# Kernel optimization log

Hardware: AMD Instinct MI355X
Metric: run time of the kernel (lower is better)

The kernel has to match this reference:

```python
import jax, jax.numpy as jnp
import numpy as np

N = 24000; E = 384000; NT = 3; IN = 128; HID = 32; ED = 64; NE = 5; FFN = 64; C = 16
HEADS = (8, 8, 1); ALPHA = 0.05; DAL = 2


def _lrelu(x, s):
    return jnp.where(x >= 0, x, s * x)


def _elu(x):
    return jnp.where(x > 0, x, jnp.expm1(x))


def _ln(x, g, b, eps=1e-5):
    m = x.mean(-1, keepdims=True)
    v = ((x - m) ** 2).mean(-1, keepdims=True)
    return (x - m) / jnp.sqrt(v + eps) * g + b


def _l2n(x, eps=1e-12):
    return x / jnp.maximum(jnp.linalg.norm(x, axis=1, keepdims=True), eps)


def _ta(h, src, dst, e_feat, edge_emb, W, We, al, ar, ae, bias, res_W, res_attn, act):
    # SimpleHGN-style heterogeneous graph attention layer (TALayer)
    Hh = al.shape[0]
    feat = (h @ W).reshape(N, Hh, HID)                       # [N,H,D]
    ee = (edge_emb[e_feat] @ We).reshape(E, Hh, ED)          # [E,H,ED]
    el = (feat * al).sum(-1)                                 # [N,H]
    er = (feat * ar).sum(-1)                                 # [N,H]
    lg = _lrelu(el[src] + er[dst] + (ee * ae).sum(-1), 0.2)  # [E,H]
    m = jax.ops.segment_max(lg, dst, num_segments=N)         # edge softmax over dst
    a = jnp.exp(lg - m[dst])
    a = a / jax.ops.segment_sum(a, dst, num_segments=N)[dst]
    if res_attn is not None:
        a = a * (1.0 - ALPHA) + res_attn * ALPHA             # residual attention carry-over
    rst = jax.ops.segment_sum(a[:, :, None] * feat[src], dst, num_segments=N)
    if res_W is not None:
        rst = rst + (h @ res_W).reshape(N, Hh, HID)
    rst = rst + bias
    if act:
        rst = _elu(rst)
    return rst, jax.lax.stop_gradient(a)


def forward(feats, fc_W, fc_b, ntype_emb, W_ntype,
            ta0_edge_emb, ta0_W, ta0_We, ta0_al, ta0_ar, ta0_ae, ta0_bias,
            ta1_edge_emb, ta1_W, ta1_We, ta1_al, ta1_ar, ta1_ae, ta1_bias, ta1_res_W,
            ta2_edge_emb, ta2_W, ta2_We, ta2_al, ta2_ar, ta2_ae, ta2_bias, ta2_res_W,
            da_ln1_g, da_ln1_b, da_Wq, da_bq, da_Wk, da_bk, da_Wv, da_bv, da_Wo, da_bo,
            da_ln2_g, da_ln2_b, da_W1, da_b1, da_W2, da_b2, final_W, logits_W,
            e_feat, node_type, src, dst):
    # per-node-type input projection + leaky_relu(0.01), concat over types -> [N,HID]
    h = _lrelu(jnp.einsum('tni,tio->tno', feats, fc_W) + fc_b[:, None, :], 0.01).reshape(N, HID)
    ntype_feat = (ntype_emb @ W_ntype)[node_type]            # [N,HID]
    h = h * ntype_feat
    h0, a0 = _ta(h, src, dst, e_feat, ta0_edge_emb, ta0_W, ta0_We, ta0_al, ta0_ar, ta0_ae, ta0_bias, None, None, True)
    h = h0.reshape(N, -1)
    h1, _ = _ta(h, src, dst, e_feat, ta1_edge_emb, ta1_W, ta1_We, ta1_al, ta1_ar, ta1_ae, ta1_bias, ta1_res_W, a0, True)
    h = h1.reshape(N, -1)
    hf, _ = _ta(h, src, dst, e_feat, ta2_edge_emb, ta2_W, ta2_We, ta2_al, ta2_ar, ta2_ae, ta2_bias, ta2_res_W, None, False)
    h_feat = hf.reshape(N, HID)
    # dim-wise transformer (DALayer stack): tokens = HID dims, channel = 1
    x = (h_feat * ntype_feat)[:, :, None]                    # [N,HID,1]
    for l in range(DAL):
        y = _ln(x, da_ln1_g[l], da_ln1_b[l])
        q = y @ da_Wq[l] + da_bq[l]
        k = y @ da_Wk[l] + da_bk[l]
        v = y @ da_Wv[l] + da_bv[l]
        att = jax.nn.softmax(jnp.einsum('nqd,nkd->nqk', q, k), axis=-1)  # scale=att_size**-0.5=1
        x = x + (jnp.einsum('nqk,nkd->nqd', att, v) @ da_Wo[l] + da_bo[l])
        y = _ln(x, da_ln2_g[l], da_ln2_b[l])
        x = x + (jax.nn.gelu(y @ da_W1[l] + da_b1[l], approximate=False) @ da_W2[l] + da_b2[l])
    h_dim = _l2n(x[:, :, 0])
    h_final = jnp.concatenate([_l2n(h_feat), h_dim], axis=1) @ final_W
    logits = jax.nn.relu(h_final) @ logits_W
    return logits / jnp.maximum(jnp.linalg.norm(logits, axis=1, keepdims=True), 1e-12)


def setup_inputs():
    key = jax.random.key(0)
    ks = iter(jax.random.split(key, 96))
    def rn(shape, s=0.1):
        return jax.random.normal(next(ks), shape, jnp.float32) * s
    inp = {}
    inp["feats"] = jax.random.normal(next(ks), (NT, N // NT, IN), jnp.float32)
    inp["e_feat"] = jax.random.randint(next(ks), (E,), 0, NE)
    inp["node_type"] = jax.random.randint(next(ks), (N,), 0, NT)
    inp["src"] = jax.random.randint(next(ks), (E,), 0, N)
    inp["dst"] = jax.random.randint(next(ks), (E,), 0, N)
    inp["fc_W"] = rn((NT, IN, HID)); inp["fc_b"] = rn((NT, HID))
    inp["ntype_emb"] = rn((NT, HID)); inp["W_ntype"] = rn((HID, HID))
    ins = (HID, HID * HEADS[0], HID * HEADS[1])
    for l in range(3):
        Hh = HEADS[l]; di = ins[l]; p = "ta%d_" % l
        inp[p + "edge_emb"] = rn((NE, ED))
        inp[p + "W"] = rn((di, Hh * HID))
        inp[p + "We"] = rn((ED, Hh * ED))
        inp[p + "al"] = rn((Hh, HID)); inp[p + "ar"] = rn((Hh, HID)); inp[p + "ae"] = rn((Hh, ED))
        inp[p + "bias"] = jnp.zeros((Hh, HID), jnp.float32)
        if l > 0:
            inp[p + "res_W"] = rn((di, Hh * HID))
    inp["da_ln1_g"] = jnp.ones((DAL, 1), jnp.float32); inp["da_ln1_b"] = jnp.zeros((DAL, 1), jnp.float32)
    inp["da_Wq"] = rn((DAL, 1, 1)); inp["da_bq"] = jnp.zeros((DAL, 1), jnp.float32)
    inp["da_Wk"] = rn((DAL, 1, 1)); inp["da_bk"] = jnp.zeros((DAL, 1), jnp.float32)
    inp["da_Wv"] = rn((DAL, 1, 1)); inp["da_bv"] = jnp.zeros((DAL, 1), jnp.float32)
    inp["da_Wo"] = rn((DAL, 1, 1)); inp["da_bo"] = jnp.zeros((DAL, 1), jnp.float32)
    inp["da_ln2_g"] = jnp.ones((DAL, 1), jnp.float32); inp["da_ln2_b"] = jnp.zeros((DAL, 1), jnp.float32)
    inp["da_W1"] = rn((DAL, 1, FFN)); inp["da_b1"] = jnp.zeros((DAL, FFN), jnp.float32)
    inp["da_W2"] = rn((DAL, FFN, 1)); inp["da_b2"] = jnp.zeros((DAL, 1), jnp.float32)
    inp["final_W"] = rn((2 * HID, HID))
    inp["logits_W"] = rn((HID, C))
    return inp


def reference(feats, fc_W, fc_b, ntype_emb, W_ntype,
              ta0_edge_emb, ta0_W, ta0_We, ta0_al, ta0_ar, ta0_ae, ta0_bias,
              ta1_edge_emb, ta1_W, ta1_We, ta1_al, ta1_ar, ta1_ae, ta1_bias, ta1_res_W,
              ta2_edge_emb, ta2_W, ta2_We, ta2_al, ta2_ar, ta2_ae, ta2_bias, ta2_res_W,
              da_ln1_g, da_ln1_b, da_Wq, da_bq, da_Wk, da_bk, da_Wv, da_bv, da_Wo, da_bo,
              da_ln2_g, da_ln2_b, da_W1, da_b1, da_W2, da_b2, final_W, logits_W,
              e_feat, node_type, src, dst):
    return forward(feats, fc_W, fc_b, ntype_emb, W_ntype,
                   ta0_edge_emb, ta0_W, ta0_We, ta0_al, ta0_ar, ta0_ae, ta0_bias,
                   ta1_edge_emb, ta1_W, ta1_We, ta1_al, ta1_ar, ta1_ae, ta1_bias, ta1_res_W,
                   ta2_edge_emb, ta2_W, ta2_We, ta2_al, ta2_ar, ta2_ae, ta2_bias, ta2_res_W,
                   da_ln1_g, da_ln1_b, da_Wq, da_bq, da_Wk, da_bk, da_Wv, da_bv, da_Wo, da_bo,
                   da_ln2_g, da_ln2_b, da_W1, da_b1, da_W2, da_b2, final_W, logits_W,
                   e_feat, node_type, src, dst)
```

## Files before the change

### kernel.cpp

```cpp
#include <hip/hip_runtime.h>
#include <math.h>

constexpr int kN = 24000;
constexpr int kE = 384000;
constexpr float kAlpha = 0.05f;

typedef unsigned int   u32;
typedef unsigned short u16;
typedef __attribute__((ext_vector_type(8))) short short8;
typedef __attribute__((ext_vector_type(4))) float float4v;

__device__ __forceinline__ float bf2f(u16 x) { return __uint_as_float(((u32)x) << 16); }
__device__ __forceinline__ u16 f2bf(float f) {
  u32 u = __float_as_uint(f);
  return (u16)((u + 0x7fffu + ((u >> 16) & 1u)) >> 16);
}

__global__ void __launch_bounds__(256) zero_ints_kernel(int* __restrict__ p, int n) {
  int i = blockIdx.x * 256 + threadIdx.x;
  if (i < n) p[i] = 0;
}

__global__ void __launch_bounds__(256) count_kernel(const int* __restrict__ dst,
                                                    int* __restrict__ counts) {
  int e = blockIdx.x * 256 + threadIdx.x;
  if (e < kE) atomicAdd(&counts[dst[e]], 1);
}

__global__ void __launch_bounds__(1024) scan_kernel(const int* __restrict__ counts,
                                                    int* __restrict__ row_start) {
  __shared__ int wsum[16];
  __shared__ int carry_s;
  int tid = threadIdx.x, lane = tid & 63, wid = tid >> 6;
  if (tid == 0) { carry_s = 0; row_start[0] = 0; }
  __syncthreads();
  for (int base = 0; base < kN; base += 1024) {
    int x = (base + tid < kN) ? counts[base + tid] : 0;
    #pragma unroll
    for (int off = 1; off < 64; off <<= 1) {
      int y = __shfl_up(x, off);
      if (lane >= off) x += y;
    }
    if (lane == 63) wsum[wid] = x;
    __syncthreads();
    if (tid < 16) {
      int wv = wsum[tid];
      #pragma unroll
      for (int off = 1; off < 16; off <<= 1) {
        int y = __shfl_up(wv, off);
        if (tid >= off) wv += y;
      }
      wsum[tid] = wv;
    }
    __syncthreads();
    int incl = x + carry_s + (wid > 0 ? wsum[wid - 1] : 0);
    if (base + tid < kN) row_start[base + tid + 1] = incl;
    __syncthreads();
    if (tid == 1023) carry_s = incl;
    __syncthreads();
  }
}

__global__ void __launch_bounds__(256) scatter_kernel(const int* __restrict__ dst,
                                                      const int* __restrict__ row_start,
                                                      int* __restrict__ cursor,
                                                      int* __restrict__ edge_ids) {
  int e = blockIdx.x * 256 + threadIdx.x;
  if (e < kE) {
    int n = dst[e];
    int pos = row_start[n] + atomicAdd(&cursor[n], 1);
    edge_ids[pos] = e;
  }
}

__global__ void __launch_bounds__(256) prepack_kernel(
    const float* __restrict__ W0, const float* __restrict__ al0, const float* __restrict__ ar0,
    const float* __restrict__ W1, const float* __restrict__ al1, const float* __restrict__ ar1,
    const float* __restrict__ rW1,
    const float* __restrict__ W2, const float* __restrict__ al2, const float* __restrict__ ar2,
    const float* __restrict__ rW2,
    u16* __restrict__ WT0, u16* __restrict__ WT1, u16* __restrict__ WT2,
    const float* __restrict__ ntype_emb, const float* __restrict__ W_ntype,
    const float* __restrict__ emb0, const float* __restrict__ We0, const float* __restrict__ ae0,
    const float* __restrict__ emb1, const float* __restrict__ We1, const float* __restrict__ ae1,
    const float* __restrict__ emb2, const float* __restrict__ We2, const float* __restrict__ ae2,
    const float* __restrict__ ln1_b, const float* __restrict__ Wv, const float* __restrict__ bv,
    const float* __restrict__ Wo, const float* __restrict__ bo,
    const float* __restrict__ ln2_b, const float* __restrict__ DW1, const float* __restrict__ Db1,
    const float* __restrict__ DW2, const float* __restrict__ Db2,
    float* __restrict__ ntf, float* __restrict__ eterm, float* __restrict__ dadelta) {
  __shared__ float wae[17][64];
  __shared__ float red[128];
  int tid = threadIdx.x;
  if (blockIdx.x < 744) {
    const int SZ0 = 10240, SZ1 = 576 * 256;
    int gid = blockIdx.x * 256 + tid;
    float v = 0.f;
    if (gid < 2048) {
      int n = gid / 32, k = gid % 32;
      if (n < 8)       { for (int d = 0; d < 32; ++d) v += W0[k * 256 + n * 32 + d] * al0[n * 32 + d]; }
      else if (n < 16) { int h = n - 8; for (int d = 0; d < 32; ++d) v += W0[k * 256 + h * 32 + d] * ar0[h * 32 + d]; }
      WT0[n * 32 + k] = f2bf(v);
    } else if (gid < SZ0) {
      int i = gid - 2048;
      int h = i >> 10, rem = i & 1023, d = rem >> 5, k = rem & 31;
      WT0[2048 + i] = f2bf(W0[k * 256 + h * 32 + d]);
    } else if (gid < SZ0 + SZ1) {
      int i = gid - SZ0;
      int n = i / 256, k = i % 256;
      if (n < 256) v = W1[k * 256 + n];
      else if (n < 264) { int h = n - 256; for (int d = 0; d < 32; ++d) v += W1[k * 256 + h * 32 + d] * al1[h * 32 + d]; }
      else if (n < 272) { int h = n - 264; for (int d = 0; d < 32; ++d) v += W1[k * 256 + h * 32 + d] * ar1[h * 32 + d]; }
      else if (n < 528) v = rW1[k * 256 + (n - 272)];
      WT1[n * 256 + k] = f2bf(v);
    } else {
      int i = gid - SZ0 - SZ1;
      int n = i / 256, k = i % 256;
      if (n < 32) v = W2[k * 32 + n];
      else if (n == 32) { for (int d = 0; d < 32; ++d) v += W2[k * 32 + d] * al2[d]; }
      else if (n == 33) { for (int d = 0; d < 32; ++d) v += W2[k * 32 + d] * ar2[d]; }
      else if (n < 66) v = rW2[k * 32 + (n - 34)];
      WT2[n * 256 + k] = f2bf(v);
    }
  } else {
    for (int idx = tid; idx < 17 * 64; idx += 256) {
      int hg = idx >> 6, k = idx & 63;
      const float* We; const float* ae; int Hh, h;
      if (hg < 8)       { We = We0; ae = ae0; Hh = 8; h = hg; }
      else if (hg < 16) { We = We1; ae = ae1; Hh = 8; h = hg - 8; }
      else              { We = We2; ae = ae2; Hh = 1; h = 0; }
      float s = 0.f;
      for (int d = 0; d < 64; ++d) s += We[(size_t)k * Hh * 64 + h * 64 + d] * ae[h * 64 + d];
      wae[hg][k] = s;
    }
    __syncthreads();
    for (int id = tid; id < 85; id += 256) {
      const float* emb; int Hh, t, h, hg, base;
      if (id < 40)      { emb = emb0; Hh = 8; t = id / 8;  h = id % 8; hg = h;      base = 0;  }
      else if (id < 80) { int i = id - 40; emb = emb1; Hh = 8; t = i / 8; h = i % 8; hg = 8 + h; base = 40; }
      else              { int i = id - 80; emb = emb2; Hh = 1; t = i;    h = 0;     hg = 16;    base = 80; }
      float s = 0.f;
      for (int k = 0; k < 64; ++k) s += emb[t * 64 + k] * wae[hg][k];
      eterm[base + t * Hh + h] = s;
    }
    for (int idx = tid; idx < 96; idx += 256) {
      int t = idx / 32, o = idx % 32;
      float s = 0.f;
      for (int k = 0; k < 32; ++k) s += ntype_emb[t * 32 + k] * W_ntype[k * 32 + o];
      ntf[idx] = s;
    }
    for (int i2 = tid; i2 < 128; i2 += 256) {
      int l = i2 >> 6, j = i2 & 63;
      float u = ln2_b[l] * DW1[l * 64 + j] + Db1[l * 64 + j];
      float g = 0.5f * u * (1.0f + erff(u * 0.7071067811865476f));
      red[i2] = g * DW2[l * 64 + j];
    }
    __syncthreads();
    if (tid == 0) {
      float delta = 0.f;
      for (int l = 0; l < 2; ++l) {
        float vs = ln1_b[l] * Wv[l] + bv[l];
        delta += vs * Wo[l] + bo[l] + Db2[l];
      }
      for (int i = 0; i < 128; ++i) delta += red[i];
      *dadelta = delta;
    }
  }
}

__global__ void __launch_bounds__(256) inproj_kernel(
    const float* __restrict__ feats, const float* __restrict__ fc_W,
    const float* __restrict__ fc_b, const float* __restrict__ ntf,
    const int* __restrict__ node_type, u16* __restrict__ hb) {
  int t = blockIdx.x * 256 + threadIdx.x;
  if (t >= kN * 32) return;
  int n = t >> 5, o = t & 31;
  int ty = n / 8000;
  const float* fr = &feats[(size_t)n * 128];
  const float* w  = &fc_W[(size_t)ty * 4096 + o];
  float s = fc_b[ty * 32 + o];
  #pragma unroll
  for (int k = 0; k < 128; k += 4) {
    float4 f = *(const float4*)&fr[k];
    s += f.x * w[(k + 0) * 32] + f.y * w[(k + 1) * 32]
       + f.z * w[(k + 2) * 32] + f.w * w[(k + 3) * 32];
  }
  s = (s < 0.f) ? 0.01f * s : s;
  hb[t] = f2bf(s * ntf[node_type[n] * 32 + o]);
}

template <int K>
__global__ void __launch_bounds__(256) mfma_gemm_kernel(
    const u16* __restrict__ A, const u16* __restrict__ WT,
    const float* __restrict__ bias,
    u16* __restrict__ featb, float* __restrict__ el, float* __restrict__ er,
    u16* __restrict__ resb, float* __restrict__ resf,
    int NT, int N1, int HH, int N2) {
  constexpr int RB = K * 2;
  constexpr int CPR = K / 8;
  __shared__ __align__(16) u16 As[64 * K];
  __shared__ __align__(16) u16 Bs[64 * K];
  const int tid = threadIdx.x;
  const int l = tid & 63;
  const int w = tid >> 6;
  const int wm = w >> 1, wn = w & 1;
  const int m0 = blockIdx.x * 64;
  const int kslot = l >> 4;
  const int l15 = l & 15;

  #pragma unroll
  for (int c = tid; c < 64 * CPR; c += 256) {
    int row = c / CPR, ch = c - row * CPR;
    int off = (row * RB + ch * 16) ^ ((row & 7) << 4);
    *(uint4*)((char*)As + off) = *(const uint4*)(A + (size_t)(m0 + row) * K + ch * 8);
  }

  for (int ct = 0; ct < NT; ++ct) {
    __syncthreads();
    #pragma unroll
    for (int c = tid; c < 64 * CPR; c += 256) {
      int row = c / CPR, ch = c - row * CPR;
      int off = (row * RB + ch * 16) ^ ((row & 7) << 4);
      *(uint4*)((char*)Bs + off) = *(const uint4*)(WT + (size_t)(ct * 64 + row) * K + ch * 8);
    }
    __syncthreads();

    float4v acc[2][2];
    #pragma unroll
    for (int f = 0; f < 2; ++f)
      #pragma unroll
      for (int g = 0; g < 2; ++g) { acc[f][g][0]=0.f; acc[f][g][1]=0.f; acc[f][g][2]=0.f; acc[f][g][3]=0.f; }

    #pragma unroll
    for (int kc = 0; kc < K; kc += 32) {
      short8 af[2], bf[2];
      #pragma unroll
      for (int f = 0; f < 2; ++f) {
        int row = wm * 32 + f * 16 + l15;
        int off = (row * RB + kc * 2 + kslot * 16) ^ ((row & 7) << 4);
        af[f] = *(const short8*)((const char*)As + off);
      }
      #pragma unroll
      for (int g = 0; g < 2; ++g) {
        int n = wn * 32 + g * 16 + l15;
        int off = (n * RB + kc * 2 + kslot * 16) ^ ((n & 7) << 4);
        bf[g] = *(const short8*)((const char*)Bs + off);
      }
      #pragma unroll
      for (int f = 0; f < 2; ++f)
        #pragma unroll
        for (int g = 0; g < 2; ++g)
          acc[f][g] = __builtin_amdgcn_mfma_f32_16x16x32_bf16(af[f], bf[g], acc[f][g], 0, 0, 0);
    }

    const int rbase = kslot * 4;
    #pragma unroll
    for (int f = 0; f < 2; ++f) {
      #pragma unroll
      for (int g = 0; g < 2; ++g) {
        int gc = ct * 64 + wn * 32 + g * 16 + l15;
        #pragma unroll
        for (int reg = 0; reg < 4; ++reg) {
          int gr = m0 + wm * 32 + f * 16 + rbase + reg;
          float v = acc[f][g][reg];
          if (gc < N1) {
            featb[(size_t)gr * N1 + gc] = f2bf(v);
          } else if (gc < N1 + HH) {
            el[(size_t)gr * HH + (gc - N1)] = v;
          } else if (gc < N1 + 2 * HH) {
            er[(size_t)gr * HH + (gc - N1 - HH)] = v;
          } else if (gc < N1 + 2 * HH + N2) {
            int c2 = gc - N1 - 2 * HH;
            float vv = v + bias[c2];
            if (resb) resb[(size_t)gr * N2 + c2] = f2bf(vv);
            else      resf[(size_t)gr * N2 + c2] = vv;
          }
        }
      }
    }
  }
}

__global__ void __launch_bounds__(256) agg8h_kernel(
    const int* __restrict__ row_start, const int* __restrict__ edge_ids,
    const int* __restrict__ src, const int* __restrict__ ef,
    const float* __restrict__ el, const float* __restrict__ er,
    const float* __restrict__ eterm,
    const u16* __restrict__ Hb,
    _Float16* __restrict__ a0h,
    u16* __restrict__ Gb) {
  int n = (blockIdx.x * 256 + threadIdx.x) >> 6;
  if (n >= kN) return;
  int l = threadIdx.x & 63;
  int h = l >> 3, s = l & 7;
  int s0 = row_start[n], s1 = row_start[n + 1];
  float ern = er[n * 8 + h];
  float et0 = eterm[0 * 8 + h], et1 = eterm[1 * 8 + h], et2 = eterm[2 * 8 + h];
  float et3 = eterm[3 * 8 + h], et4 = eterm[4 * 8 + h];
  float m = -1e30f, ssum = 0.f;
  for (int i = s0 + s; i < s1; i += 8) {
    int e = edge_ids[i];
    int efc = ef[e];
    float etv = (efc == 0) ? et0 : (efc == 1) ? et1 : (efc == 2) ? et2 : (efc == 3) ? et3 : et4;
    float lg = el[src[e] * 8 + h] + ern + etv;
    lg = (lg < 0.f) ? 0.2f * lg : lg;
    if (lg > m) { ssum = ssum * expf(m - lg) + 1.f; m = lg; }
    else        { ssum += expf(lg - m); }
  }
  #pragma unroll
  for (int mk = 1; mk <= 4; mk <<= 1) {
    float om = __shfl_xor(m, mk);
    float os = __shfl_xor(ssum, mk);
    float nm = fmaxf(m, om);
    ssum = ssum * expf(m - nm) + os * expf(om - nm);
    m = nm;
  }
  float inv = 1.f / ssum;
  float4 acc = make_float4(0.f, 0.f, 0.f, 0.f);
  int i = s0;
  for (; i + 8 <= s1; i += 8) {
    int e = edge_ids[i + s];
    int sek = src[e];
    int efc = ef[e];
    float etv = (efc == 0) ? et0 : (efc == 1) ? et1 : (efc == 2) ? et2 : (efc == 3) ? et3 : et4;
    float lg = el[sek * 8 + h] + ern + etv;
    lg = (lg < 0.f) ? 0.2f * lg : lg;
    float am = expf(lg - m) * inv;
    a0h[(size_t)e * 8 + h] = (_Float16)am;
    #pragma unroll
    for (int j = 0; j < 8; ++j) {
      float aj = __shfl(am, (h << 3) + j);
      int sej = __shfl(sek, j);
      ushort4 fv = *(const ushort4*)(Hb + (size_t)sej * 32 + s * 4);
      acc.x = fmaf(aj, bf2f(fv.x), acc.x);
      acc.y = fmaf(aj, bf2f(fv.y), acc.y);
      acc.z = fmaf(aj, bf2f(fv.z), acc.z);
      acc.w = fmaf(aj, bf2f(fv.w), acc.w);
    }
  }
  if (i < s1) {
    int cnt = s1 - i;
    float am = 0.f; int sek = 0;
    if (s < cnt) {
      int e = edge_ids[i + s];
      sek = src[e];
      int efc = ef[e];
      float etv = (efc == 0) ? et0 : (efc == 1) ? et1 : (efc == 2) ? et2 : (efc == 3) ? et3 : et4;
      float lg = el[sek * 8 + h] + ern + etv;
      lg = (lg < 0.f) ? 0.2f * lg : lg;
      am = expf(lg - m) * inv;
      a0h[(size_t)e * 8 + h] = (_Float16)am;
    }
    for (int j = 0; j < cnt; ++j) {
      float aj = __shfl(am, (h << 3) + j);
      int sej = __shfl(sek, j);
      ushort4 fv = *(const ushort4*)(Hb + (size_t)sej * 32 + s * 4);
      acc.x = fmaf(aj, bf2f(fv.x), acc.x);
      acc.y = fmaf(aj, bf2f(fv.y), acc.y);
      acc.z = fmaf(aj, bf2f(fv.z), acc.z);
      acc.w = fmaf(aj, bf2f(fv.w), acc.w);
    }
  }
  ushort4 pw;
  pw.x = f2bf(acc.x); pw.y = f2bf(acc.y); pw.z = f2bf(acc.z); pw.w = f2bf(acc.w);
  *(ushort4*)(Gb + (size_t)n * 256 + h * 32 + s * 4) = pw;
}

__global__ void __launch_bounds__(256) bd_gemm_kernel(
    const u16* __restrict__ Gb,
    const u16* __restrict__ WbdT,
    const float* __restrict__ bias,
    u16* __restrict__ outb) {
  __shared__ __align__(16) u16 As[64 * 256];
  __shared__ __align__(16) u16 Bs[8 * 32 * 32];
  const int tid = threadIdx.x;
  const int l = tid & 63;
  const int w = tid >> 6;
  const int m0 = blockIdx.x * 64;
  const int kslot = l >> 4, l15 = l & 15;
  for (int c = tid; c < 64 * 32; c += 256) {
    int row = c >> 5, ch = c & 31;
    int off = (row * 512 + ch * 16) ^ ((row & 7) << 4);
    *(uint4*)((char*)As + off) = *(const uint4*)(Gb + (size_t)(m0 + row) * 256 + ch * 8);
  }
  for (int c = tid; c < 256 * 4; c += 256) {
    int r = c >> 2, ch = c & 3;
    int off = (r * 64 + ch * 16) ^ ((r & 7) << 4);
    *(uint4*)((char*)Bs + off) = *(const uint4*)(WbdT + (size_t)r * 32 + ch * 8);
  }
  __syncthreads();
  #pragma unroll
  for (int hh = 0; hh < 2; ++hh) {
    int h = w * 2 + hh;
    short8 af[4];
    #pragma unroll
    for (int f = 0; f < 4; ++f) {
      int row = f * 16 + l15;
      int off = (row * 512 + h * 64 + kslot * 16) ^ ((row & 7) << 4);
      af[f] = *(const short8*)((const char*)As + off);
    }
    short8 bf[2];
    #pragma unroll
    for (int g = 0; g < 2; ++g) {
      int r = h * 32 + g * 16 + l15;
      int off = (r * 64 + kslot * 16) ^ ((r & 7) << 4);
      bf[g] = *(const short8*)((const char*)Bs + off);
    }
    #pragma unroll
    for (int f = 0; f < 4; ++f) {
      #pragma unroll
      for (int g = 0; g < 2; ++g) {
        float4v acc = {0.f, 0.f, 0.f, 0.f};
        acc = __builtin_amdgcn_mfma_f32_16x16x32_bf16(af[f], bf[g], acc, 0, 0, 0);
        #pragma unroll
        for (int reg = 0; reg < 4; ++reg) {
          int gr = m0 + f * 16 + kslot * 4 + reg;
          int gc = h * 32 + g * 16 + l15;
          float v = acc[reg] + bias[gc];
          v = (v > 0.f) ? v : expm1f(v);
          outb[(size_t)gr * 256 + gc] = f2bf(v);
        }
      }
    }
  }
}

__global__ void __launch_bounds__(256) agg8w_kernel(
    const int* __restrict__ row_start, const int* __restrict__ edge_ids,
    const int* __restrict__ src, const int* __restrict__ ef,
    const float* __restrict__ el, const float* __restrict__ er,
    const float* __restrict__ eterm,
    const u16* __restrict__ featb,
    const _Float16* __restrict__ a0h,
    const u16* __restrict__ accb,
    u16* __restrict__ outb) {
  int n = (blockIdx.x * 256 + threadIdx.x) >> 6;
  if (n >= kN) return;
  int l = threadIdx.x & 63;
  int h = l >> 3, s = l & 7;
  int s0 = row_start[n], s1 = row_start[n + 1];
  float ern = er[n * 8 + h];
  float et0 = eterm[0 * 8 + h], et1 = eterm[1 * 8 + h], et2 = eterm[2 * 8 + h];
  float et3 = eterm[3 * 8 + h], et4 = eterm[4 * 8 + h];
  float m = -1e30f, ssum = 0.f;
  for (int i = s0 + s; i < s1; i += 8) {
    int e = edge_ids[i];
    int efc = ef[e];
    float etv = (efc == 0) ? et0 : (efc == 1) ? et1 : (efc == 2) ? et2 : (efc == 3) ? et3 : et4;
    float lg = el[src[e] * 8 + h] + ern + etv;
    lg = (lg < 0.f) ? 0.2f * lg : lg;
    if (lg > m) { ssum = ssum * expf(m - lg) + 1.f; m = lg; }
    else        { ssum += expf(lg - m); }
  }
  #pragma unroll
  for (int mk = 1; mk <= 4; mk <<= 1) {
    float om = __shfl_xor(m, mk);
    float os = __shfl_xor(ssum, mk);
    float nm = fmaxf(m, om);
    ssum = ssum * expf(m - nm) + os * expf(om - nm);
    m = nm;
  }
  float inv = 1.f / ssum;
  const size_t rowoff = (size_t)n * 256 + h * 32 + s * 4;
  ushort4 rv = *(const ushort4*)(accb + rowoff);
  float4 acc = make_float4(bf2f(rv.x), bf2f(rv.y), bf2f(rv.z), bf2f(rv.w));
  int i = s0;
  for (; i + 8 <= s1; i += 8) {
    int e = edge_ids[i + s];
    int sek = src[e];
    int efc = ef[e];
    float etv = (efc == 0) ? et0 : (efc == 1) ? et1 : (efc == 2) ? et2 : (efc == 3) ? et3 : et4;
    float lg = el[sek * 8 + h] + ern + etv;
    lg = (lg < 0.f) ? 0.2f * lg : lg;
    float am = expf(lg - m) * inv;
    am = am * (1.f - kAlpha) + (float)a0h[(size_t)e * 8 + h] * kAlpha;
    #pragma unroll
    for (int j = 0; j < 8; ++j) {
      float aj = __shfl(am, (h << 3) + j);
      int sej = __shfl(sek, j);
      ushort4 fv = *(const ushort4*)(featb + (size_t)sej * 256 + h * 32 + s * 4);
      acc.x = fmaf(aj, bf2f(fv.x), acc.x);
      acc.y = fmaf(aj, bf2f(fv.y), acc.y);
      acc.z = fmaf(aj, bf2f(fv.z), acc.z);
      acc.w = fmaf(aj, bf2f(fv.w), acc.w);
    }
  }
  if (i < s1) {
    int cnt = s1 - i;
    float am = 0.f; int sek = 0;
    if (s < cnt) {
      int e = edge_ids[i + s];
      sek = src[e];
      int efc = ef[e];
      float etv = (efc == 0) ? et0 : (efc == 1) ? et1 : (efc == 2) ? et2 : (efc == 3) ? et3 : et4;
      float lg = el[sek * 8 + h] + ern + etv;
      lg = (lg < 0.f) ? 0.2f * lg : lg;
      am = expf(lg - m) * inv;
      am = am * (1.f - kAlpha) + (float)a0h[(size_t)e * 8 + h] * kAlpha;
    }
    for (int j = 0; j < cnt; ++j) {
      float aj = __shfl(am, (h << 3) + j);
      int sej = __shfl(sek, j);
      ushort4 fv = *(const ushort4*)(featb + (size_t)sej * 256 + h * 32 + s * 4);
      acc.x = fmaf(aj, bf2f(fv.x), acc.x);
      acc.y = fmaf(aj, bf2f(fv.y), acc.y);
      acc.z = fmaf(aj, bf2f(fv.z), acc.z);
      acc.w = fmaf(aj, bf2f(fv.w), acc.w);
    }
  }
  acc.x = (acc.x > 0.f) ? acc.x : expm1f(acc.x);
  acc.y = (acc.y > 0.f) ? acc.y : expm1f(acc.y);
  acc.z = (acc.z > 0.f) ? acc.z : expm1f(acc.z);
  acc.w = (acc.w > 0.f) ? acc.w : expm1f(acc.w);
  ushort4 pw;
  pw.x = f2bf(acc.x); pw.y = f2bf(acc.y); pw.z = f2bf(acc.z); pw.w = f2bf(acc.w);
  *(ushort4*)(outb + rowoff) = pw;
}

__global__ void __launch_bounds__(256) aggw1_final_kernel(
    const int* __restrict__ row_start, const int* __restrict__ edge_ids,
    const int* __restrict__ src, const int* __restrict__ ef,
    const float* __restrict__ el, const float* __restrict__ er,
    const float* __restrict__ eterm,
    const u16* __restrict__ featb,
    const float* __restrict__ S2,
    const float* __restrict__ ntf, const int* __restrict__ node_type,
    const float* __restrict__ dadelta,
    const float* __restrict__ finalW, const float* __restrict__ logitsW,
    float* __restrict__ out) {
  __shared__ float fWs[2048];
  __shared__ float lWs[512];
  __shared__ float abuf[8][32];
  __shared__ float bbuf[8][32];
  __shared__ float sbuf[8][32];
  const int tid = threadIdx.x;
  for (int i = tid; i < 2048; i += 256) fWs[i] = finalW[i];
  for (int i = tid; i < 512; i += 256) lWs[i] = logitsW[i];
  const int slot = tid >> 5;
  const int g = tid & 31;
  const int gb = tid & 32;
  const int n = blockIdx.x * 8 + slot;
  const int s0 = row_start[n], s1 = row_start[n + 1];
  float ern = er[n];
  float et0 = eterm[0], et1 = eterm[1], et2 = eterm[2], et3 = eterm[3], et4 = eterm[4];
  float m = -1e30f, ssum = 0.f;
  for (int i = s0 + g; i < s1; i += 32) {
    int e = edge_ids[i];
    int efc = ef[e];
    float etv = (efc == 0) ? et0 : (efc == 1) ? et1 : (efc == 2) ? et2 : (efc == 3) ? et3 : et4;
    float lg = el[src[e]] + ern + etv;
    lg = (lg < 0.f) ? 0.2f * lg : lg;
    if (lg > m) { ssum = ssum * expf(m - lg) + 1.f; m = lg; }
    else        { ssum += expf(lg - m); }
  }
  #pragma unroll
  for (int mk = 1; mk <= 16; mk <<= 1) {
    float om = __shfl_xor(m, mk);
    float os = __shfl_xor(ssum, mk);
    float nm = fmaxf(m, om);
    ssum = ssum * expf(m - nm) + os * expf(om - nm);
    m = nm;
  }
  float inv = 1.f / ssum;
  float acc = S2[(size_t)n * 32 + g];
  int i = s0;
  for (; i + 32 <= s1; i += 32) {
    int e = edge_ids[i + g];
    int sek = src[e];
    int efc = ef[e];
    float etv = (efc == 0) ? et0 : (efc == 1) ? et1 : (efc == 2) ? et2 : (efc == 3) ? et3 : et4;
    float lg = el[sek] + ern + etv;
    lg = (lg < 0.f) ? 0.2f * lg : lg;
    float am = expf(lg - m) * inv;
    #pragma unroll
    for (int j = 0; j < 32; ++j) {
      float aj = __shfl(am, gb + j);
      int sej = __shfl(sek, gb + j);
      acc = fmaf(aj, bf2f(featb[(size_t)sej * 32 + g]), acc);
    }
  }
  if (i < s1) {
    int cnt = s1 - i;
    float am = 0.f; int sek = 0;
    if (g < cnt) {
      int e = edge_ids[i + g];
      sek = src[e];
      int efc = ef[e];
      float etv = (efc == 0) ? et0 : (efc == 1) ? et1 : (efc == 2) ? et2 : (efc == 3) ? et3 : et4;
      float lg = el[sek] + ern + etv;
      lg = (lg < 0.f) ? 0.2f * lg : lg;
      am = expf(lg - m) * inv;
    }
    for (int j = 0; j < cnt; ++j) {
      float aj = __shfl(am, gb + j);
      int sej = __shfl(sek, gb + j);
      acc = fmaf(aj, bf2f(featb[(size_t)sej * 32 + g]), acc);
    }
  }
  float delta = dadelta[0];
  float ntv = ntf[node_type[n] * 32 + g];
  float av = acc;
  float bv = acc * ntv + delta;
  float na = av * av, nb = bv * bv;
  #pragma unroll
  for (int mk = 1; mk <= 16; mk <<= 1) {
    na += __shfl_xor(na, mk);
    nb += __shfl_xor(nb, mk);
  }
  float inva = 1.f / fmaxf(sqrtf(na), 1e-12f);
  float invb = 1.f / fmaxf(sqrtf(nb), 1e-12f);
  __syncthreads();
  abuf[slot][g] = av * inva;
  bbuf[slot][g] = bv * invb;
  __syncthreads();
  float s = 0.f;
  #pragma unroll
  for (int d = 0; d < 32; ++d)
    s += abuf[slot][d] * fWs[d * 32 + g] + bbuf[slot][d] * fWs[(32 + d) * 32 + g];
  s = fmaxf(s, 0.f);
  sbuf[slot][g] = s;
  __syncthreads();
  if (g < 16) {
    float lg = 0.f;
    #pragma unroll
    for (int o = 0; o < 32; ++o) lg += sbuf[slot][o] * lWs[o * 16 + g];
    float nl = lg * lg;
    #pragma unroll
    for (int mk = 1; mk <= 8; mk <<= 1) nl += __shfl_xor(nl, mk);
    float invl = 1.f / fmaxf(sqrtf(nl), 1e-12f);
    out[(size_t)n * 16 + g] = lg * invl;
  }
}

extern "C" void kernel_launch(void* const* d_in, const int* in_sizes, int n_in,
                              void* d_out, int out_size, void* d_ws, size_t ws_size,
                              hipStream_t stream) {
  const float* feats     = (const float*)d_in[0];
  const int*   e_feat    = (const int*)d_in[1];
  const int*   node_type = (const int*)d_in[2];
  const int*   src       = (const int*)d_in[3];
  const int*   dst       = (const int*)d_in[4];
  const float* fc_W      = (const float*)d_in[5];
  const float* fc_b      = (const float*)d_in[6];
  const float* ntype_emb = (const float*)d_in[7];
  const float* W_ntype   = (const float*)d_in[8];
  const float* ta_edge_emb[3] = {(const float*)d_in[9],  (const float*)d_in[16], (const float*)d_in[24]};
  const float* ta_W[3]        = {(const float*)d_in[10], (const float*)d_in[17], (const float*)d_in[25]};
  const float* ta_We[3]       = {(const float*)d_in[11], (const float*)d_in[18], (const float*)d_in[26]};
  const float* ta_al[3]       = {(const float*)d_in[12], (const float*)d_in[19], (const float*)d_in[27]};
  const float* ta_ar[3]       = {(const float*)d_in[13], (const float*)d_in[20], (const float*)d_in[28]};
  const float* ta_ae[3]       = {(const float*)d_in[14], (const float*)d_in[21], (const float*)d_in[29]};
  const float* ta_bias[3]     = {(const float*)d_in[15], (const float*)d_in[22], (const float*)d_in[30]};
  const float* ta1_res_W = (const float*)d_in[23];
  const float* ta2_res_W = (const float*)d_in[31];
  const float* da_ln1_b  = (const float*)d_in[33];
  const float* da_Wv     = (const float*)d_in[38];
  const float* da_bv     = (const float*)d_in[39];
  const float* da_Wo     = (const float*)d_in[40];
  const float* da_bo     = (const float*)d_in[41];
  const float* da_ln2_b  = (const float*)d_in[43];
  const float* da_W1     = (const float*)d_in[44];
  const float* da_b1     = (const float*)d_in[45];
  const float* da_W2     = (const float*)d_in[46];
  const float* da_b2     = (const float*)d_in[47];
  const float* final_W   = (const float*)d_in[48];
  const float* logits_W  = (const float*)d_in[49];
  float* out = (float*)d_out;

  char* base = (char*)d_ws;
  int* iws       = (int*)base;
  int* counts    = iws;
  int* cursor    = iws + kN;
  int* row_start = iws + 2 * kN;
  int* edge_ids  = iws + 2 * kN + kN + 1;
  char* p = base + (size_t)456004 * 4;
  float* ntf = (float*)p;                     p += 512;
  float* etm = (float*)p;                     p += 512;
  float* dad = (float*)p;                     p += 64;
  float* el  = (float*)p;                     p += (size_t)kN * 8 * 4;
  float* er  = (float*)p;                     p += (size_t)kN * 8 * 4;
  float* S2  = (float*)p;                     p += (size_t)kN * 32 * 4;
  u16*   Hb  = (u16*)p;                       p += (size_t)kN * 32 * 2;
  _Float16* a0h = (_Float16*)p;               p += (size_t)kE * 8 * 2;
  u16* featb = (u16*)p;                       p += (size_t)kN * 256 * 2;
  u16* Rb0   = (u16*)p;                       p += (size_t)kN * 256 * 2;
  u16* Rpr   = (u16*)p;                       p += (size_t)kN * 256 * 2;
  u16* WT0   = (u16*)p;                       p += (size_t)320 * 32 * 2;
  u16* WT1   = (u16*)p;                       p += (size_t)576 * 256 * 2;
  u16* WT2   = (u16*)p;                       p += (size_t)128 * 256 * 2;
  u16* WT0el = WT0;
  u16* Wbd0T = WT0 + 2048;

  zero_ints_kernel<<<(2 * kN + 255) / 256, 256, 0, stream>>>(counts, 2 * kN);
  count_kernel<<<kE / 256, 256, 0, stream>>>(dst, counts);
  scan_kernel<<<1, 1024, 0, stream>>>(counts, row_start);
  scatter_kernel<<<kE / 256, 256, 0, stream>>>(dst, row_start, cursor, edge_ids);

  prepack_kernel<<<745, 256, 0, stream>>>(
      ta_W[0], ta_al[0], ta_ar[0],
      ta_W[1], ta_al[1], ta_ar[1], ta1_res_W,
      ta_W[2], ta_al[2], ta_ar[2], ta2_res_W,
      WT0, WT1, WT2,
      ntype_emb, W_ntype,
      ta_edge_emb[0], ta_We[0], ta_ae[0],
      ta_edge_emb[1], ta_We[1], ta_ae[1],
      ta_edge_emb[2], ta_We[2], ta_ae[2],
      da_ln1_b, da_Wv, da_bv, da_Wo, da_bo,
      da_ln2_b, da_W1, da_b1, da_W2, da_b2,
      ntf, etm, dad);

  inproj_kernel<<<(kN * 32) / 256, 256, 0, stream>>>(feats, fc_W, fc_b, ntf, node_type, Hb);

  mfma_gemm_kernel<32><<<kN / 64, 256, 0, stream>>>(
      Hb, WT0el, nullptr, nullptr, el, er, nullptr, nullptr, 1, 0, 8, 0);
  agg8h_kernel<<<kN / 4, 256, 0, stream>>>(
      row_start, edge_ids, src, e_feat, el, er, etm, Hb, a0h, featb);
  bd_gemm_kernel<<<kN / 64, 256, 0, stream>>>(featb, Wbd0T, ta_bias[0], Rb0);

  mfma_gemm_kernel<256><<<kN / 64, 256, 0, stream>>>(
      Rb0, WT1, ta_bias[1], featb, el, er, Rpr, nullptr, 9, 256, 8, 256);
  agg8w_kernel<<<kN / 4, 256, 0, stream>>>(
      row_start, edge_ids, src, e_feat, el, er, etm + 40, featb, a0h, Rpr, Rpr);

  mfma_gemm_kernel<256><<<kN / 64, 256, 0, stream>>>(
      Rpr, WT2, ta_bias[2], featb, el, er, nullptr, S2, 2, 32, 1, 32);
  aggw1_final_kernel<<<kN / 8, 256, 0, stream>>>(
      row_start, edge_ids, src, e_feat, el, er, etm + 80, featb, S2,
      ntf, node_type, dad, final_W, logits_W, out);
}
```

Measured before the change: 490.0 us.

## Replace serial scan with atomic wave allocation and split GEMM column tiles across blocks

Replaces the single-block prefix scan with a parallel per-wave scan that reserves segment bases via a global atomic, so CSR segments are contiguous but in arbitrary order; aggregation kernels now use counts to find segment ends. The MFMA GEMM kernels get a 2D grid that distributes column tiles across blocks to raise parallelism. This removes a serialized single-block stage and under-filled GEMM launches, at the cost of redundant A-tile loads and less sequential edge-segment layout.

```diff
diff --git a/kernel.cpp b/kernel.cpp
--- a/kernel.cpp
+++ b/kernel.cpp
@@ -27,38 +27,23 @@
   if (e < kE) atomicAdd(&counts[dst[e]], 1);
 }
 
-__global__ void __launch_bounds__(1024) scan_kernel(const int* __restrict__ counts,
+__global__ void __launch_bounds__(256) alloc_kernel(const int* __restrict__ counts,
+                                                    int* __restrict__ gcur,
                                                     int* __restrict__ row_start) {
-  __shared__ int wsum[16];
-  __shared__ int carry_s;
-  int tid = threadIdx.x, lane = tid & 63, wid = tid >> 6;
-  if (tid == 0) { carry_s = 0; row_start[0] = 0; }
-  __syncthreads();
-  for (int base = 0; base < kN; base += 1024) {
-    int x = (base + tid < kN) ? counts[base + tid] : 0;
-    #pragma unroll
-    for (int off = 1; off < 64; off <<= 1) {
-      int y = __shfl_up(x, off);
-      if (lane >= off) x += y;
-    }
-    if (lane == 63) wsum[wid] = x;
-    __syncthreads();
-    if (tid < 16) {
-      int wv = wsum[tid];
-      #pragma unroll
-      for (int off = 1; off < 16; off <<= 1) {
-        int y = __shfl_up(wv, off);
-        if (tid >= off) wv += y;
-      }
-      wsum[tid] = wv;
-    }
-    __syncthreads();
-    int incl = x + carry_s + (wid > 0 ? wsum[wid - 1] : 0);
-    if (base + tid < kN) row_start[base + tid + 1] = incl;
-    __syncthreads();
-    if (tid == 1023) carry_s = incl;
-    __syncthreads();
-  }
+  int t = blockIdx.x * 256 + threadIdx.x;
+  int lane = threadIdx.x & 63;
+  int c = (t < kN) ? counts[t] : 0;
+  int x = c;
+  #pragma unroll
+  for (int off = 1; off < 64; off <<= 1) {
+    int y = __shfl_up(x, off);
+    if (lane >= off) x += y;
+  }
+  int wtotal = __shfl(x, 63);
+  int base = 0;
+  if (lane == 63) base = atomicAdd(gcur, wtotal);
+  base = __shfl(base, 63);
+  if (t < kN) row_start[t] = base + x - c;
 }
 
 __global__ void __launch_bounds__(256) scatter_kernel(const int* __restrict__ dst,
@@ -195,7 +180,7 @@
     const float* __restrict__ bias,
     u16* __restrict__ featb, float* __restrict__ el, float* __restrict__ er,
     u16* __restrict__ resb, float* __restrict__ resf,
-    int NT, int N1, int HH, int N2) {
+    int tpb, int N1, int HH, int N2) {
   constexpr int RB = K * 2;
   constexpr int CPR = K / 8;
   __shared__ __align__(16) u16 As[64 * K];
@@ -204,7 +189,7 @@
   const int l = tid & 63;
   const int w = tid >> 6;
   const int wm = w >> 1, wn = w & 1;
-  const int m0 = blockIdx.x * 64;
+  const int m0 = blockIdx.y * 64;
   const int kslot = l >> 4;
   const int l15 = l & 15;
 
@@ -215,7 +200,8 @@
     *(uint4*)((char*)As + off) = *(const uint4*)(A + (size_t)(m0 + row) * K + ch * 8);
   }
 
-  for (int ct = 0; ct < NT; ++ct) {
+  for (int t = 0; t < tpb; ++t) {
+    int ct = blockIdx.x * tpb + t;
     __syncthreads();
     #pragma unroll
     for (int c = tid; c < 64 * CPR; c += 256) {
@@ -282,7 +268,8 @@
 }
 
 __global__ void __launch_bounds__(256) agg8h_kernel(
-    const int* __restrict__ row_start, const int* __restrict__ edge_ids,
+    const int* __restrict__ row_start, const int* __restrict__ counts,
+    const int* __restrict__ edge_ids,
     const int* __restrict__ src, const int* __restrict__ ef,
     const float* __restrict__ el, const float* __restrict__ er,
     const float* __restrict__ eterm,
@@ -293,7 +280,7 @@
   if (n >= kN) return;
   int l = threadIdx.x & 63;
   int h = l >> 3, s = l & 7;
-  int s0 = row_start[n], s1 = row_start[n + 1];
+  int s0 = row_start[n], s1 = s0 + counts[n];
   float ern = er[n * 8 + h];
   float et0 = eterm[0 * 8 + h], et1 = eterm[1 * 8 + h], et2 = eterm[2 * 8 + h];
   float et3 = eterm[3 * 8 + h], et4 = eterm[4 * 8 + h];
@@ -367,10 +354,8 @@
 }
 
 __global__ void __launch_bounds__(256) bd_gemm_kernel(
-    const u16* __restrict__ Gb,
-    const u16* __restrict__ WbdT,
-    const float* __restrict__ bias,
-    u16* __restrict__ outb) {
+    const u16* __restrict__ Gb, const u16* __restrict__ WbdT,
+    const float* __restrict__ bias, u16* __restrict__ outb) {
   __shared__ __align__(16) u16 As[64 * 256];
   __shared__ __align__(16) u16 Bs[8 * 32 * 32];
   const int tid = threadIdx.x;
@@ -426,7 +411,8 @@
 }
 
 __global__ void __launch_bounds__(256) agg8w_kernel(
-    const int* __restrict__ row_start, const int* __restrict__ edge_ids,
+    const int* __restrict__ row_start, const int* __restrict__ counts,
+    const int* __restrict__ edge_ids,
     const int* __restrict__ src, const int* __restrict__ ef,
     const float* __restrict__ el, const float* __restrict__ er,
     const float* __restrict__ eterm,
@@ -438,7 +424,7 @@
   if (n >= kN) return;
   int l = threadIdx.x & 63;
   int h = l >> 3, s = l & 7;
-  int s0 = row_start[n], s1 = row_start[n + 1];
+  int s0 = row_start[n], s1 = s0 + counts[n];
   float ern = er[n * 8 + h];
   float et0 = eterm[0 * 8 + h], et1 = eterm[1 * 8 + h], et2 = eterm[2 * 8 + h];
   float et3 = eterm[3 * 8 + h], et4 = eterm[4 * 8 + h];
@@ -518,7 +504,8 @@
 }
 
 __global__ void __launch_bounds__(256) aggw1_final_kernel(
-    const int* __restrict__ row_start, const int* __restrict__ edge_ids,
+    const int* __restrict__ row_start, const int* __restrict__ counts,
+    const int* __restrict__ edge_ids,
     const int* __restrict__ src, const int* __restrict__ ef,
     const float* __restrict__ el, const float* __restrict__ er,
     const float* __restrict__ eterm,
@@ -540,7 +527,7 @@
   const int g = tid & 31;
   const int gb = tid & 32;
   const int n = blockIdx.x * 8 + slot;
-  const int s0 = row_start[n], s1 = row_start[n + 1];
+  const int s0 = row_start[n], s1 = s0 + counts[n];
   float ern = er[n];
   float et0 = eterm[0], et1 = eterm[1], et2 = eterm[2], et3 = eterm[3], et4 = eterm[4];
   float m = -1e30f, ssum = 0.f;
@@ -671,8 +658,9 @@
   int* iws       = (int*)base;
   int* counts    = iws;
   int* cursor    = iws + kN;
-  int* row_start = iws + 2 * kN;
-  int* edge_ids  = iws + 2 * kN + kN + 1;
+  int* gcur      = iws + 2 * kN;
+  int* row_start = iws + 2 * kN + 4;
+  int* edge_ids  = iws + 3 * kN + 4;
   char* p = base + (size_t)456004 * 4;
   float* ntf = (float*)p;                     p += 512;
   float* etm = (float*)p;                     p += 512;
@@ -691,9 +679,9 @@
   u16* WT0el = WT0;
   u16* Wbd0T = WT0 + 2048;
 
-  zero_ints_kernel<<<(2 * kN + 255) / 256, 256, 0, stream>>>(counts, 2 * kN);
+  zero_ints_kernel<<<(2 * kN + 4 + 255) / 256, 256, 0, stream>>>(counts, 2 * kN + 4);
   count_kernel<<<kE / 256, 256, 0, stream>>>(dst, counts);
-  scan_kernel<<<1, 1024, 0, stream>>>(counts, row_start);
+  alloc_kernel<<<(kN + 255) / 256, 256, 0, stream>>>(counts, gcur, row_start);
   scatter_kernel<<<kE / 256, 256, 0, stream>>>(dst, row_start, cursor, edge_ids);
 
   prepack_kernel<<<745, 256, 0, stream>>>(
@@ -711,20 +699,21 @@
 
   inproj_kernel<<<(kN * 32) / 256, 256, 0, stream>>>(feats, fc_W, fc_b, ntf, node_type, Hb);
 
-  mfma_gemm_kernel<32><<<kN / 64, 256, 0, stream>>>(
+  mfma_gemm_kernel<32><<<dim3(1, kN / 64), 256, 0, stream>>>(
       Hb, WT0el, nullptr, nullptr, el, er, nullptr, nullptr, 1, 0, 8, 0);
   agg8h_kernel<<<kN / 4, 256, 0, stream>>>(
-      row_start, edge_ids, src, e_feat, el, er, etm, Hb, a0h, featb);
+      row_start, counts, edge_ids, src, e_feat, el, er, etm, Hb, a0h, featb);
   bd_gemm_kernel<<<kN / 64, 256, 0, stream>>>(featb, Wbd0T, ta_bias[0], Rb0);
 
-  mfma_gemm_kernel<256><<<kN / 64, 256, 0, stream>>>(
-      Rb0, WT1, ta_bias[1], featb, el, er, Rpr, nullptr, 9, 256, 8, 256);
+  mfma_gemm_kernel<256><<<dim3(3, kN / 64), 256, 0, stream>>>(
+      Rb0, WT1, ta_bias[1], featb, el, er, Rpr, nullptr, 3, 256, 8, 256);
   agg8w_kernel<<<kN / 4, 256, 0, stream>>>(
-      row_start, edge_ids, src, e_feat, el, er, etm + 40, featb, a0h, Rpr, Rpr);
-
-  mfma_gemm_kernel<256><<<kN / 64, 256, 0, stream>>>(
-      Rpr, WT2, ta_bias[2], featb, el, er, nullptr, S2, 2, 32, 1, 32);
+      row_start, counts, edge_ids, src, e_feat, el, er, etm + 40,
+      featb, a0h, Rpr, Rpr);
+
+  mfma_gemm_kernel<256><<<dim3(2, kN / 64), 256, 0, stream>>>(
+      Rpr, WT2, ta_bias[2], featb, el, er, nullptr, S2, 1, 32, 1, 32);
   aggw1_final_kernel<<<kN / 8, 256, 0, stream>>>(
-      row_start, edge_ids, src, e_feat, el, er, etm + 80, featb, S2,
+      row_start, counts, edge_ids, src, e_feat, el, er, etm + 80, featb, S2,
       ntf, node_type, dad, final_W, logits_W, out);
 }
```

New measurement: 483.7 us. Within noise of the previous version (-1.3%).
